# Optimization experiments

Measured on AMD Instinct MI355X. Metric: run time of the kernel, lower is better.

The kernel has to match this reference:

```python
import jax, jax.numpy as jnp
import numpy as np

B, T, D = 2, 2048, 1024
H, HD = 16, 64
MAX_LEN = 2048


def setup_inputs() -> dict:
    key = jax.random.key(0)
    ks = jax.random.split(key, 7)
    s = 0.02
    return {
        "x": jax.random.normal(ks[0], (B, T, D), dtype=jnp.float32),
        "qkv_w": jax.random.normal(ks[1], (3 * D, D), dtype=jnp.float32) * s,
        "qkv_b": jax.random.normal(ks[2], (3 * D,), dtype=jnp.float32) * s,
        "out_w": jax.random.normal(ks[3], (D, D), dtype=jnp.float32) * s,
        "out_b": jax.random.normal(ks[4], (D,), dtype=jnp.float32) * s,
        "rel_pos": jax.random.normal(ks[5], (2 * MAX_LEN - 1, HD), dtype=jnp.float32),
        "rpe_w": jax.random.normal(ks[6], (HD,), dtype=jnp.float32) * s,
    }


def reference(x, qkv_w, qkv_b, out_w, out_b, rel_pos, rpe_w):
    Bq, Tq, Dq = x.shape
    scale = HD ** -0.5
    qkv = x @ qkv_w.T + qkv_b  # [B,T,3D]
    qkv = qkv.reshape(Bq, Tq, 3, H, HD)
    q = qkv[:, :, 0].transpose(0, 2, 1, 3)  # [B,H,T,HD]
    k = qkv[:, :, 1].transpose(0, 2, 1, 3)
    v = qkv[:, :, 2].transpose(0, 2, 1, 3)
    scores = jnp.einsum('bhqd,bhkd->bhqk', q, k) * scale  # [B,H,T,T]
    # relative position bias: gather rel embeddings, project to scalar
    rel_idx = jnp.arange(Tq)[None, :] - jnp.arange(Tq)[:, None] + MAX_LEN - 1  # [T,T]
    bias = (rel_pos @ rpe_w)[rel_idx]  # project first (cheap), then gather -> [T,T]
    scores = scores + bias[None, None]
    attn = jax.nn.softmax(scores, axis=-1)
    out = jnp.einsum('bhqk,bhkd->bhqd', attn, v)  # [B,H,T,HD]
    out = out.transpose(0, 2, 1, 3).reshape(Bq, Tq, Dq)
    return out @ out_w.T + out_b
```

## Files before the change

kernel.cpp:

```cpp
#include <hip/hip_runtime.h>
#include <math.h>

#define B_ 2
#define T_ 2048
#define D_ 1024
#define H_ 16
#define HD_ 64
#define MAXLEN_ 2048
#define N3D_ 3072
#define M_ (B_ * T_)
#define KA 1024

#define SCALE_L2E 0.18033688011116215f
#define L2E 1.4426950408889634f

typedef unsigned short ushort_t;
typedef __attribute__((ext_vector_type(8))) short short8;
typedef __attribute__((ext_vector_type(4))) float floatx4;
#define MFMA16(a, b, c) __builtin_amdgcn_mfma_f32_16x16x32_bf16(a, b, c, 0, 0, 0)

static __device__ __forceinline__ ushort_t f2bf(float f) {
    unsigned u = __float_as_uint(f);
    unsigned r = (u + 0x7FFFu + ((u >> 16) & 1u)) >> 16;
    return (ushort_t)r;
}
static __device__ __forceinline__ unsigned pack2bf(float a, float b) {
    unsigned ua = __float_as_uint(a), ub = __float_as_uint(b);
    ua = ua + 0x7FFFu + ((ua >> 16) & 1u);
    ub = ub + 0x7FFFu + ((ub >> 16) & 1u);
    return (ua >> 16) | (ub & 0xFFFF0000u);
}

static __device__ __forceinline__ void gld16(const ushort_t* g, ushort_t* l) {
    __builtin_amdgcn_global_load_lds(
        (const __attribute__((address_space(1))) void*)g,
        (__attribute__((address_space(3))) void*)l, 16, 0, 0);
}

__global__ __launch_bounds__(256) void cvt_all(
    const float* __restrict__ x, const float* __restrict__ qw,
    const float* __restrict__ ow,
    ushort_t* __restrict__ Xc, ushort_t* __restrict__ QWc,
    ushort_t* __restrict__ OWc)
{
    const int row = blockIdx.x;
    const float* src; ushort_t* dst; int r;
    if (row < M_)            { src = x;  dst = Xc;  r = row; }
    else if (row < M_ + N3D_){ src = qw; dst = QWc; r = row - M_; }
    else                     { src = ow; dst = OWc; r = row - M_ - N3D_; }
    const int c = threadIdx.x * 4;
    float4 v = *(const float4*)(src + (size_t)r * 1024 + c);
    ushort4 hv;
    hv.x = f2bf(v.x); hv.y = f2bf(v.y); hv.z = f2bf(v.z); hv.w = f2bf(v.w);
    *(ushort4*)(dst + (size_t)r * KA + c) = hv;
}

__global__ __launch_bounds__(256) void qkv_mfma(
    const ushort_t* __restrict__ Ac, const ushort_t* __restrict__ Bc,
    const float* __restrict__ bias,
    ushort_t* __restrict__ Qs, ushort_t* __restrict__ Khi,
    ushort_t* __restrict__ Vt)
{
    __shared__ __align__(16) ushort_t As[16 * 512];
    __shared__ __align__(16) ushort_t Bs[16 * 512];
    const int tid = threadIdx.x;
    const int wv = tid >> 6, lane = tid & 63;
    const int l16 = lane & 15, quad = lane >> 4;
    const int wm = wv & 1, wn = wv >> 1;
    const int m0 = blockIdx.y * 128, n0 = blockIdx.x * 128;

    floatx4 acc[4][4];
#pragma unroll
    for (int i = 0; i < 4; ++i)
#pragma unroll
        for (int j = 0; j < 4; ++j) acc[i][j] = (floatx4){0.f, 0.f, 0.f, 0.f};

    for (int k0 = 0; k0 < KA; k0 += 64) {
        __syncthreads();
#pragma unroll
        for (int c = 0; c < 4; ++c) {
            const int b = wv * 4 + c;
            const int i = b >> 1, ks = b & 1;
            const int k = k0 + ks * 32 + quad * 8;
            gld16(Ac + (size_t)(m0 + i * 16 + l16) * KA + k, As + b * 512);
            gld16(Bc + (size_t)(n0 + i * 16 + l16) * KA + k, Bs + b * 512);
        }
        __syncthreads();
#pragma unroll
        for (int ks = 0; ks < 2; ++ks) {
            short8 af[4], bf[4];
#pragma unroll
            for (int ii = 0; ii < 4; ++ii)
                af[ii] = *(const short8*)(As + ((wm * 4 + ii) * 2 + ks) * 512 + lane * 8);
#pragma unroll
            for (int jj = 0; jj < 4; ++jj)
                bf[jj] = *(const short8*)(Bs + ((wn * 4 + jj) * 2 + ks) * 512 + lane * 8);
#pragma unroll
            for (int ii = 0; ii < 4; ++ii)
#pragma unroll
                for (int jj = 0; jj < 4; ++jj)
                    acc[ii][jj] = MFMA16(af[ii], bf[jj], acc[ii][jj]);
        }
    }

#pragma unroll
    for (int ii = 0; ii < 4; ++ii) {
#pragma unroll
        for (int r = 0; r < 4; ++r) {
            const int m = m0 + wm * 64 + ii * 16 + quad * 4 + r;
            const int bb = m >> 11, t = m & 2047;
#pragma unroll
            for (int jj = 0; jj < 4; ++jj) {
                const int n = n0 + wn * 64 + jj * 16 + l16;
                const int c = n >> 10, h = (n >> 6) & 15, hd = n & 63;
                const float v = acc[ii][jj][r] + bias[n];
                const size_t idx = (((size_t)bb * H_ + h) * T_ + t) * HD_ + hd;
                if (c == 0) { Qs[idx] = f2bf(v * SCALE_L2E); }
                else if (c == 1) { Khi[idx] = f2bf(v); }
                else { Vt[(((size_t)bb * H_ + h) * HD_ + hd) * T_ + t] = f2bf(v); }
            }
        }
    }
}

__global__ __launch_bounds__(256) void out_mfma(
    const ushort_t* __restrict__ Ac, const ushort_t* __restrict__ Bc,
    const float* __restrict__ bias, float* __restrict__ Out)
{
    __shared__ __align__(16) ushort_t As[16 * 512];
    __shared__ __align__(16) ushort_t Bs[8 * 512];
    const int tid = threadIdx.x;
    const int wv = tid >> 6, lane = tid & 63;
    const int l16 = lane & 15, quad = lane >> 4;
    const int wm = wv & 1, wn = wv >> 1;
    const int m0 = blockIdx.y * 128, n0 = blockIdx.x * 64;

    floatx4 acc[4][2];
#pragma unroll
    for (int i = 0; i < 4; ++i)
#pragma unroll
        for (int j = 0; j < 2; ++j) acc[i][j] = (floatx4){0.f, 0.f, 0.f, 0.f};

    for (int k0 = 0; k0 < KA; k0 += 64) {
        __syncthreads();
#pragma unroll
        for (int c = 0; c < 4; ++c) {
            const int b = wv * 4 + c;
            const int i = b >> 1, ks = b & 1;
            const int k = k0 + ks * 32 + quad * 8;
            gld16(Ac + (size_t)(m0 + i * 16 + l16) * KA + k, As + b * 512);
        }
#pragma unroll
        for (int c = 0; c < 2; ++c) {
            const int b = wv * 2 + c;
            const int j = b >> 1, ks = b & 1;
            const int k = k0 + ks * 32 + quad * 8;
            gld16(Bc + (size_t)(n0 + j * 16 + l16) * KA + k, Bs + b * 512);
        }
        __syncthreads();
#pragma unroll
        for (int ks = 0; ks < 2; ++ks) {
            short8 af[4], bf[2];
#pragma unroll
            for (int ii = 0; ii < 4; ++ii)
                af[ii] = *(const short8*)(As + ((wm * 4 + ii) * 2 + ks) * 512 + lane * 8);
#pragma unroll
            for (int jj = 0; jj < 2; ++jj)
                bf[jj] = *(const short8*)(Bs + ((wn * 2 + jj) * 2 + ks) * 512 + lane * 8);
#pragma unroll
            for (int ii = 0; ii < 4; ++ii)
#pragma unroll
                for (int jj = 0; jj < 2; ++jj)
                    acc[ii][jj] = MFMA16(af[ii], bf[jj], acc[ii][jj]);
        }
    }

#pragma unroll
    for (int ii = 0; ii < 4; ++ii) {
#pragma unroll
        for (int r = 0; r < 4; ++r) {
            const int m = m0 + wm * 64 + ii * 16 + quad * 4 + r;
#pragma unroll
            for (int jj = 0; jj < 2; ++jj) {
                const int n = n0 + wn * 32 + jj * 16 + l16;
                Out[(size_t)m * D_ + n] = acc[ii][jj][r] + bias[n];
            }
        }
    }
}

__global__ __launch_bounds__(64) void rpe_project(
    const float* __restrict__ rel_pos, const float* __restrict__ rpe_w,
    float* __restrict__ biasp)
{
    const int i = blockIdx.x;
    const int lane = threadIdx.x;
    float v = rel_pos[(size_t)i * HD_ + lane] * rpe_w[lane];
#pragma unroll
    for (int off = 32; off; off >>= 1) v += __shfl_down(v, off);
    if (lane == 0) biasp[i] = v * L2E;
}

__global__ __launch_bounds__(256) void attn_mfma(
    const ushort_t* __restrict__ Qs, const ushort_t* __restrict__ Khi,
    const ushort_t* __restrict__ Vt, const float* __restrict__ biasp,
    ushort_t* __restrict__ AOc)
{
    __shared__ __align__(16) ushort_t KS[2][8 * 512];
    __shared__ __align__(16) ushort_t VS[2][8 * 512];
    __shared__ __align__(16) ushort_t PS[4][2 * 512];

    const int i = blockIdx.x;
    const int bh = (i & 7) + 8 * (i >> 8);
    const int q0 = ((i >> 3) & 31) * 64;
    const int tid = threadIdx.x;
    const int wv = tid >> 6, lane = tid & 63;
    const int l16 = lane & 15, quad = lane >> 4;

    const int q = q0 + wv * 16 + l16;
    const size_t qoff = ((size_t)bh * T_ + q) * HD_ + quad * 8;
    const short8 qh0 = *(const short8*)(Qs + qoff);
    const short8 qh1 = *(const short8*)(Qs + qoff + 32);

    float l_r = 0.f;
    floatx4 o_acc[4];
#pragma unroll
    for (int g2 = 0; g2 < 4; ++g2) o_acc[g2] = (floatx4){0.f, 0.f, 0.f, 0.f};

    const ushort_t* gK = Khi + (size_t)bh * T_ * HD_;
    const ushort_t* gV = Vt + (size_t)bh * HD_ * T_;
    const int biasbase = 2047 + quad * 4 - q;

    const int qdbase = quad >> 1;
    ushort_t* pw = PS[wv];

    const size_t kstage = (size_t)(wv * 16 + l16) * HD_ + quad * 8;
    const size_t vstage = (size_t)(wv * 16 + l16) * T_ + quad * 8;

    gld16(gK + kstage,              KS[0] + (wv * 2 + 0) * 512);
    gld16(gK + kstage + 32,         KS[0] + (wv * 2 + 1) * 512);
    gld16(gV + vstage,              VS[0] + (wv * 2 + 0) * 512);
    gld16(gV + vstage + 32,         VS[0] + (wv * 2 + 1) * 512);
    __syncthreads();

    for (int t = 0; t < 32; ++t) {
        const int k0 = t * 64;
        const int buf = t & 1, nbuf = buf ^ 1;

        if (t < 31) {
            const size_t koff = kstage + (size_t)(k0 + 64) * HD_;
            gld16(gK + koff,      KS[nbuf] + (wv * 2 + 0) * 512);
            gld16(gK + koff + 32, KS[nbuf] + (wv * 2 + 1) * 512);
            const size_t voff = vstage + (size_t)(k0 + 64);
            gld16(gV + voff,      VS[nbuf] + (wv * 2 + 0) * 512);
            gld16(gV + voff + 32, VS[nbuf] + (wv * 2 + 1) * 512);
        }
        float4 bb[4];
#pragma unroll
        for (int g = 0; g < 4; ++g)
            __builtin_memcpy(&bb[g], biasp + (biasbase + k0 + g * 16), 16);

#pragma unroll
        for (int g = 0; g < 4; ++g) {
            const short8 kh0 = *(const short8*)(KS[buf] + (g * 2 + 0) * 512 + lane * 8);
            const short8 kh1 = *(const short8*)(KS[buf] + (g * 2 + 1) * 512 + lane * 8);
            floatx4 a = (floatx4){0.f, 0.f, 0.f, 0.f};
            a = MFMA16(kh0, qh0, a);
            a = MFMA16(kh1, qh1, a);
            const float* bp = (const float*)&bb[g];
            float p0 = __builtin_amdgcn_exp2f(a[0] + bp[0]);
            float p1 = __builtin_amdgcn_exp2f(a[1] + bp[1]);
            float p2 = __builtin_amdgcn_exp2f(a[2] + bp[2]);
            float p3 = __builtin_amdgcn_exp2f(a[3] + bp[3]);
            l_r += (p0 + p1) + (p2 + p3);
            uint2 pkd;
            pkd.x = pack2bf(p0, p1);
            pkd.y = pack2bf(p2, p3);
            const int qd = 2 * (g & 1) + qdbase;
            *(uint2*)(pw + (g >> 1) * 512 + (qd * 16 + l16) * 8 + (quad & 1) * 4) = pkd;
        }
        const short8 p0 = *(const short8*)(pw + lane * 8);
        const short8 p1 = *(const short8*)(pw + 512 + lane * 8);

#pragma unroll
        for (int g2 = 0; g2 < 4; ++g2) {
            const short8 v0 = *(const short8*)(VS[buf] + (g2 * 2 + 0) * 512 + lane * 8);
            const short8 v1 = *(const short8*)(VS[buf] + (g2 * 2 + 1) * 512 + lane * 8);
            o_acc[g2] = MFMA16(v0, p0, o_acc[g2]);
            o_acc[g2] = MFMA16(v1, p1, o_acc[g2]);
        }
        __syncthreads();
    }

    l_r += __shfl_xor(l_r, 16);
    l_r += __shfl_xor(l_r, 32);
    const float inv = 1.0f / l_r;
    const int bb2 = bh >> 4, h2 = bh & 15;
    const size_t m = (size_t)bb2 * T_ + q;
#pragma unroll
    for (int g2 = 0; g2 < 4; ++g2) {
        uint2 pk;
        pk.x = pack2bf(o_acc[g2][0] * inv, o_acc[g2][1] * inv);
        pk.y = pack2bf(o_acc[g2][2] * inv, o_acc[g2][3] * inv);
        *(uint2*)(AOc + m * KA + h2 * 64 + g2 * 16 + quad * 4) = pk;
    }
}

extern "C" void kernel_launch(void* const* d_in, const int* in_sizes, int n_in,
                              void* d_out, int out_size, void* d_ws, size_t ws_size,
                              hipStream_t stream)
{
    const float* x       = (const float*)d_in[0];
    const float* qkv_w   = (const float*)d_in[1];
    const float* qkv_b   = (const float*)d_in[2];
    const float* out_w   = (const float*)d_in[3];
    const float* out_b   = (const float*)d_in[4];
    const float* rel_pos = (const float*)d_in[5];
    const float* rpe_w   = (const float*)d_in[6];
    float* out = (float*)d_out;

    const size_t QE = (size_t)B_ * H_ * T_ * HD_;
    ushort_t* Qs  = (ushort_t*)d_ws;
    ushort_t* Khi = Qs  + QE;
    ushort_t* Vt  = Khi + QE;
    ushort_t* Xc  = Vt  + QE;
    ushort_t* QWc = Xc  + (size_t)M_ * KA;
    ushort_t* OWc = QWc + (size_t)N3D_ * KA;
    ushort_t* AOc = OWc + (size_t)D_ * KA;
    float* biasp  = (float*)(AOc + (size_t)M_ * KA);

    cvt_all<<<M_ + N3D_ + D_, 256, 0, stream>>>(x, qkv_w, out_w, Xc, QWc, OWc);
    rpe_project<<<2 * MAXLEN_ - 1, 64, 0, stream>>>(rel_pos, rpe_w, biasp);

    qkv_mfma<<<dim3(N3D_ / 128, M_ / 128), 256, 0, stream>>>(
        Xc, QWc, qkv_b, Qs, Khi, Vt);
    attn_mfma<<<1024, 256, 0, stream>>>(Qs, Khi, Vt, biasp, AOc);
    out_mfma<<<dim3(D_ / 64, M_ / 128), 256, 0, stream>>>(
        AOc, OWc, out_b, out);
}
```

Baseline: 278.0 us.

## Double per-wave query rows in attention, fuse RPE projection, cheaper bf16 pack

The attention kernel now has each wave handle 32 query rows instead of 16, so every K/V tile staged in LDS feeds twice as many MFMAs. The block count drops from 1024 to 512 and register use rises. The relative-position projection moves into the conversion kernel as extra blocks, which removes one launch. The bf16 packing switches from round-to-nearest-even to round-half-up using a byte permute, which uses fewer ALU ops but changes rounding slightly.

```diff
diff --git a/kernel.cpp b/kernel.cpp
--- a/kernel.cpp
+++ b/kernel.cpp
@@ -24,11 +24,10 @@
     unsigned r = (u + 0x7FFFu + ((u >> 16) & 1u)) >> 16;
     return (ushort_t)r;
 }
-static __device__ __forceinline__ unsigned pack2bf(float a, float b) {
-    unsigned ua = __float_as_uint(a), ub = __float_as_uint(b);
-    ua = ua + 0x7FFFu + ((ua >> 16) & 1u);
-    ub = ub + 0x7FFFu + ((ub >> 16) & 1u);
-    return (ua >> 16) | (ub & 0xFFFF0000u);
+static __device__ __forceinline__ unsigned packrnu(float a, float b) {
+    unsigned ua = __float_as_uint(a) + 0x8000u;
+    unsigned ub = __float_as_uint(b) + 0x8000u;
+    return __builtin_amdgcn_perm(ub, ua, 0x07060302u);
 }
 
 static __device__ __forceinline__ void gld16(const ushort_t* g, ushort_t* l) {
@@ -39,20 +38,32 @@
 
 __global__ __launch_bounds__(256) void cvt_all(
     const float* __restrict__ x, const float* __restrict__ qw,
-    const float* __restrict__ ow,
+    const float* __restrict__ ow, const float* __restrict__ rel_pos,
+    const float* __restrict__ rpe_w,
     ushort_t* __restrict__ Xc, ushort_t* __restrict__ QWc,
-    ushort_t* __restrict__ OWc)
+    ushort_t* __restrict__ OWc, float* __restrict__ biasp)
 {
     const int row = blockIdx.x;
-    const float* src; ushort_t* dst; int r;
-    if (row < M_)            { src = x;  dst = Xc;  r = row; }
-    else if (row < M_ + N3D_){ src = qw; dst = QWc; r = row - M_; }
-    else                     { src = ow; dst = OWc; r = row - M_ - N3D_; }
-    const int c = threadIdx.x * 4;
-    float4 v = *(const float4*)(src + (size_t)r * 1024 + c);
-    ushort4 hv;
-    hv.x = f2bf(v.x); hv.y = f2bf(v.y); hv.z = f2bf(v.z); hv.w = f2bf(v.w);
-    *(ushort4*)(dst + (size_t)r * KA + c) = hv;
+    if (row < M_ + N3D_ + D_) {
+        const float* src; ushort_t* dst; int r;
+        if (row < M_)            { src = x;  dst = Xc;  r = row; }
+        else if (row < M_ + N3D_){ src = qw; dst = QWc; r = row - M_; }
+        else                     { src = ow; dst = OWc; r = row - M_ - N3D_; }
+        const int c = threadIdx.x * 4;
+        float4 v = *(const float4*)(src + (size_t)r * 1024 + c);
+        ushort4 hv;
+        hv.x = f2bf(v.x); hv.y = f2bf(v.y); hv.z = f2bf(v.z); hv.w = f2bf(v.w);
+        *(ushort4*)(dst + (size_t)r * KA + c) = hv;
+    } else {
+        const int wv = threadIdx.x >> 6, lane = threadIdx.x & 63;
+        const int r = (row - (M_ + N3D_ + D_)) * 4 + wv;
+        if (r < 2 * MAXLEN_ - 1) {
+            float v = rel_pos[(size_t)r * HD_ + lane] * rpe_w[lane];
+#pragma unroll
+            for (int off = 32; off; off >>= 1) v += __shfl_down(v, off);
+            if (lane == 0) biasp[r] = v * L2E;
+        }
+    }
 }
 
 __global__ __launch_bounds__(256) void qkv_mfma(
@@ -189,18 +200,6 @@
     }
 }
 
-__global__ __launch_bounds__(64) void rpe_project(
-    const float* __restrict__ rel_pos, const float* __restrict__ rpe_w,
-    float* __restrict__ biasp)
-{
-    const int i = blockIdx.x;
-    const int lane = threadIdx.x;
-    float v = rel_pos[(size_t)i * HD_ + lane] * rpe_w[lane];
-#pragma unroll
-    for (int off = 32; off; off >>= 1) v += __shfl_down(v, off);
-    if (lane == 0) biasp[i] = v * L2E;
-}
-
 __global__ __launch_bounds__(256) void attn_mfma(
     const ushort_t* __restrict__ Qs, const ushort_t* __restrict__ Khi,
     const ushort_t* __restrict__ Vt, const float* __restrict__ biasp,
@@ -208,39 +207,46 @@
 {
     __shared__ __align__(16) ushort_t KS[2][8 * 512];
     __shared__ __align__(16) ushort_t VS[2][8 * 512];
-    __shared__ __align__(16) ushort_t PS[4][2 * 512];
+    __shared__ __align__(16) ushort_t PS[4][2][1024];
 
     const int i = blockIdx.x;
-    const int bh = (i & 7) + 8 * (i >> 8);
-    const int q0 = ((i >> 3) & 31) * 64;
+    const int j = i >> 3;
+    const int bh = (i & 7) + 8 * (j >> 4);
+    const int q0 = (j & 15) * 128;
     const int tid = threadIdx.x;
     const int wv = tid >> 6, lane = tid & 63;
     const int l16 = lane & 15, quad = lane >> 4;
 
-    const int q = q0 + wv * 16 + l16;
-    const size_t qoff = ((size_t)bh * T_ + q) * HD_ + quad * 8;
-    const short8 qh0 = *(const short8*)(Qs + qoff);
-    const short8 qh1 = *(const short8*)(Qs + qoff + 32);
-
-    float l_r = 0.f;
-    floatx4 o_acc[4];
-#pragma unroll
-    for (int g2 = 0; g2 < 4; ++g2) o_acc[g2] = (floatx4){0.f, 0.f, 0.f, 0.f};
+    const int qw = q0 + wv * 32;
+
+    short8 qh[2][2];
+#pragma unroll
+    for (int u = 0; u < 2; ++u) {
+        const size_t qoff = ((size_t)bh * T_ + qw + u * 16 + l16) * HD_ + quad * 8;
+        qh[u][0] = *(const short8*)(Qs + qoff);
+        qh[u][1] = *(const short8*)(Qs + qoff + 32);
+    }
+
+    float l_r[2] = {0.f, 0.f};
+    floatx4 o_acc[4][2];
+#pragma unroll
+    for (int g2 = 0; g2 < 4; ++g2)
+#pragma unroll
+        for (int u = 0; u < 2; ++u) o_acc[g2][u] = (floatx4){0.f, 0.f, 0.f, 0.f};
 
     const ushort_t* gK = Khi + (size_t)bh * T_ * HD_;
     const ushort_t* gV = Vt + (size_t)bh * HD_ * T_;
-    const int biasbase = 2047 + quad * 4 - q;
-
+    const int bias_u[2] = {2047 + quad * 4 - (qw + l16),
+                           2047 + quad * 4 - (qw + 16 + l16)};
     const int qdbase = quad >> 1;
-    ushort_t* pw = PS[wv];
 
     const size_t kstage = (size_t)(wv * 16 + l16) * HD_ + quad * 8;
     const size_t vstage = (size_t)(wv * 16 + l16) * T_ + quad * 8;
 
-    gld16(gK + kstage,              KS[0] + (wv * 2 + 0) * 512);
-    gld16(gK + kstage + 32,         KS[0] + (wv * 2 + 1) * 512);
-    gld16(gV + vstage,              VS[0] + (wv * 2 + 0) * 512);
-    gld16(gV + vstage + 32,         VS[0] + (wv * 2 + 1) * 512);
+    gld16(gK + kstage,      KS[0] + (wv * 2 + 0) * 512);
+    gld16(gK + kstage + 32, KS[0] + (wv * 2 + 1) * 512);
+    gld16(gV + vstage,      VS[0] + (wv * 2 + 0) * 512);
+    gld16(gV + vstage + 32, VS[0] + (wv * 2 + 1) * 512);
     __syncthreads();
 
     for (int t = 0; t < 32; ++t) {
@@ -255,54 +261,65 @@
             gld16(gV + voff,      VS[nbuf] + (wv * 2 + 0) * 512);
             gld16(gV + voff + 32, VS[nbuf] + (wv * 2 + 1) * 512);
         }
-        float4 bb[4];
-#pragma unroll
-        for (int g = 0; g < 4; ++g)
-            __builtin_memcpy(&bb[g], biasp + (biasbase + k0 + g * 16), 16);
 
 #pragma unroll
         for (int g = 0; g < 4; ++g) {
             const short8 kh0 = *(const short8*)(KS[buf] + (g * 2 + 0) * 512 + lane * 8);
             const short8 kh1 = *(const short8*)(KS[buf] + (g * 2 + 1) * 512 + lane * 8);
-            floatx4 a = (floatx4){0.f, 0.f, 0.f, 0.f};
-            a = MFMA16(kh0, qh0, a);
-            a = MFMA16(kh1, qh1, a);
-            const float* bp = (const float*)&bb[g];
-            float p0 = __builtin_amdgcn_exp2f(a[0] + bp[0]);
-            float p1 = __builtin_amdgcn_exp2f(a[1] + bp[1]);
-            float p2 = __builtin_amdgcn_exp2f(a[2] + bp[2]);
-            float p3 = __builtin_amdgcn_exp2f(a[3] + bp[3]);
-            l_r += (p0 + p1) + (p2 + p3);
-            uint2 pkd;
-            pkd.x = pack2bf(p0, p1);
-            pkd.y = pack2bf(p2, p3);
             const int qd = 2 * (g & 1) + qdbase;
-            *(uint2*)(pw + (g >> 1) * 512 + (qd * 16 + l16) * 8 + (quad & 1) * 4) = pkd;
-        }
-        const short8 p0 = *(const short8*)(pw + lane * 8);
-        const short8 p1 = *(const short8*)(pw + 512 + lane * 8);
+#pragma unroll
+            for (int u = 0; u < 2; ++u) {
+                floatx4 a = (floatx4){0.f, 0.f, 0.f, 0.f};
+                a = MFMA16(kh0, qh[u][0], a);
+                a = MFMA16(kh1, qh[u][1], a);
+                float4 bb;
+                __builtin_memcpy(&bb, biasp + (bias_u[u] + k0 + g * 16), 16);
+                const float p0 = __builtin_amdgcn_exp2f(a[0] + bb.x);
+                const float p1 = __builtin_amdgcn_exp2f(a[1] + bb.y);
+                const float p2 = __builtin_amdgcn_exp2f(a[2] + bb.z);
+                const float p3 = __builtin_amdgcn_exp2f(a[3] + bb.w);
+                l_r[u] += (p0 + p1) + (p2 + p3);
+                uint2 pkd;
+                pkd.x = packrnu(p0, p1);
+                pkd.y = packrnu(p2, p3);
+                *(uint2*)(PS[wv][u] + (g >> 1) * 512 + (qd * 16 + l16) * 8 + (quad & 1) * 4) = pkd;
+            }
+        }
+
+        short8 pf[2][2];
+#pragma unroll
+        for (int u = 0; u < 2; ++u) {
+            pf[u][0] = *(const short8*)(PS[wv][u] + lane * 8);
+            pf[u][1] = *(const short8*)(PS[wv][u] + 512 + lane * 8);
+        }
 
 #pragma unroll
         for (int g2 = 0; g2 < 4; ++g2) {
             const short8 v0 = *(const short8*)(VS[buf] + (g2 * 2 + 0) * 512 + lane * 8);
             const short8 v1 = *(const short8*)(VS[buf] + (g2 * 2 + 1) * 512 + lane * 8);
-            o_acc[g2] = MFMA16(v0, p0, o_acc[g2]);
-            o_acc[g2] = MFMA16(v1, p1, o_acc[g2]);
-        }
-        __syncthreads();
-    }
-
-    l_r += __shfl_xor(l_r, 16);
-    l_r += __shfl_xor(l_r, 32);
-    const float inv = 1.0f / l_r;
+#pragma unroll
+            for (int u = 0; u < 2; ++u) {
+                o_acc[g2][u] = MFMA16(v0, pf[u][0], o_acc[g2][u]);
+                o_acc[g2][u] = MFMA16(v1, pf[u][1], o_acc[g2][u]);
+            }
+        }
+        __syncthreads();
+    }
+
     const int bb2 = bh >> 4, h2 = bh & 15;
-    const size_t m = (size_t)bb2 * T_ + q;
-#pragma unroll
-    for (int g2 = 0; g2 < 4; ++g2) {
-        uint2 pk;
-        pk.x = pack2bf(o_acc[g2][0] * inv, o_acc[g2][1] * inv);
-        pk.y = pack2bf(o_acc[g2][2] * inv, o_acc[g2][3] * inv);
-        *(uint2*)(AOc + m * KA + h2 * 64 + g2 * 16 + quad * 4) = pk;
+#pragma unroll
+    for (int u = 0; u < 2; ++u) {
+        l_r[u] += __shfl_xor(l_r[u], 16);
+        l_r[u] += __shfl_xor(l_r[u], 32);
+        const float inv = 1.0f / l_r[u];
+        const size_t m = (size_t)bb2 * T_ + qw + u * 16 + l16;
+#pragma unroll
+        for (int g2 = 0; g2 < 4; ++g2) {
+            uint2 pk;
+            pk.x = packrnu(o_acc[g2][u][0] * inv, o_acc[g2][u][1] * inv);
+            pk.y = packrnu(o_acc[g2][u][2] * inv, o_acc[g2][u][3] * inv);
+            *(uint2*)(AOc + m * KA + h2 * 64 + g2 * 16 + quad * 4) = pk;
+        }
     }
 }
 
@@ -329,12 +346,12 @@
     ushort_t* AOc = OWc + (size_t)D_ * KA;
     float* biasp  = (float*)(AOc + (size_t)M_ * KA);
 
-    cvt_all<<<M_ + N3D_ + D_, 256, 0, stream>>>(x, qkv_w, out_w, Xc, QWc, OWc);
-    rpe_project<<<2 * MAXLEN_ - 1, 64, 0, stream>>>(rel_pos, rpe_w, biasp);
+    cvt_all<<<M_ + N3D_ + D_ + 1024, 256, 0, stream>>>(
+        x, qkv_w, out_w, rel_pos, rpe_w, Xc, QWc, OWc, biasp);
 
     qkv_mfma<<<dim3(N3D_ / 128, M_ / 128), 256, 0, stream>>>(
         Xc, QWc, qkv_b, Qs, Khi, Vt);
-    attn_mfma<<<1024, 256, 0, stream>>>(Qs, Khi, Vt, biasp, AOc);
+    attn_mfma<<<512, 256, 0, stream>>>(Qs, Khi, Vt, biasp, AOc);
     out_mfma<<<dim3(D_ / 64, M_ / 128), 256, 0, stream>>>(
         AOc, OWc, out_b, out);
 }
```

New measurement: 272.5 us. Within noise of the previous version (-2.0%).
